# Optimization experiments

Measured on AMD Instinct MI355X. Metric: run time of the kernel, lower is better.

The kernel has to match this reference:

```python
import jax, jax.numpy as jnp
import numpy as np

B, H, N, D = 4, 16, 4096, 64
M = 266  # nb_features = int(D * ln(D))
KERNEL_EPS = 1e-4


def _gaussian_orthogonal_random_matrix(nb_rows, nb_cols, rng):
    # Faithful to gaussian_orthogonal_random_matrix with scaling=0.
    blocks = []
    for _ in range(nb_rows // nb_cols):
        q, _ = np.linalg.qr(rng.standard_normal((nb_cols, nb_cols)))
        blocks.append(q.T)
    rem = nb_rows - (nb_rows // nb_cols) * nb_cols
    if rem > 0:
        q, _ = np.linalg.qr(rng.standard_normal((nb_cols, nb_cols)))
        blocks.append(q.T[:rem])
    final = np.concatenate(blocks, axis=0)
    mult = np.linalg.norm(rng.standard_normal((nb_rows, nb_cols)), axis=1)
    return (mult[:, None] * final).astype(np.float32)


def setup_inputs() -> dict:
    key = jax.random.key(0)
    kq, kk, kv = jax.random.split(key, 3)
    q = jax.random.normal(kq, (B, H, N, D), dtype=jnp.float32)
    k = jax.random.normal(kk, (B, H, N, D), dtype=jnp.float32)
    v = jax.random.normal(kv, (B, H, N, D), dtype=jnp.float32)
    proj = jnp.asarray(_gaussian_orthogonal_random_matrix(M, D, np.random.default_rng(0)))
    return {"q": q, "k": k, "v": v, "projection_matrix": proj}


def _softmax_kernel(x, proj, is_query):
    d = x.shape[-1]
    data_normalizer = d ** (-0.25)
    ratio = proj.shape[0] ** (-0.5)
    # [b,h,n,m]
    data_dash = jnp.einsum("bhnd,md->bhnm", data_normalizer * x, proj)
    diag = jnp.sum(x * x, axis=-1, keepdims=True) * 0.5 * (data_normalizer ** 2)
    if is_query:
        mx = jax.lax.stop_gradient(jnp.max(data_dash, axis=-1, keepdims=True))
    else:
        mx = jax.lax.stop_gradient(jnp.max(data_dash, axis=(-1, -2), keepdims=True))
    return ratio * (jnp.exp(data_dash - diag - mx) + KERNEL_EPS)


def _linear_attention(q, k, v):
    k_cumsum = jnp.sum(k, axis=-2)                       # [b,h,m]
    D_ = jnp.einsum("bhnm,bhm->bhn", q, k_cumsum)
    D_inv = 1.0 / jnp.where(D_ == 0, 1e-5, D_)
    context = jnp.einsum("bhnm,bhne->bhme", k, v)        # [b,h,m,e]
    return jnp.einsum("bhme,bhnm,bhn->bhne", context, q, D_inv)


def reference(q, k, v, projection_matrix):
    qp = _softmax_kernel(q, projection_matrix, is_query=True)
    kp = _softmax_kernel(k, projection_matrix, is_query=False)
    return _linear_attention(qp, kp, v)
```

## Files before the change

kernel.cpp:

```cpp
#include <hip/hip_runtime.h>
#include <math.h>


#define BH 64
#define NTOK 4096
#define DIM 64
#define MF 266
#define MPAD 272
#define NCH 4
#define CHROWS 1024
#define SUBS 16
#define RATIO 0.06131393394849658f
#define DNORM 0.35355339059327373f
#define DIAGC 0.0625f
#define KEPS 1e-4f

#define PSTR 72
#define QSTR 296

typedef _Float16 half8 __attribute__((ext_vector_type(8)));
typedef _Float16 half4 __attribute__((ext_vector_type(4)));
typedef __fp16 fp16x2 __attribute__((ext_vector_type(2)));
typedef float floatx4 __attribute__((ext_vector_type(4)));
typedef short short8 __attribute__((ext_vector_type(8)));
typedef short short4s __attribute__((ext_vector_type(4)));

__device__ __forceinline__ short f2h_bits(float f) {
    union { _Float16 h; short s; } u; u.h = (_Float16)f; return u.s;
}
__device__ __forceinline__ float h2f(short s) {
    union { short s; _Float16 h; } u; u.s = s; return (float)u.h;
}
__device__ __forceinline__ unsigned cvt_pk_bf16(float lo, float hi) {
    unsigned r;
    asm("v_cvt_pk_bf16_f32 %0, %1, %2" : "=v"(r) : "v"(lo), "v"(hi));
    return r;
}
__device__ __forceinline__ unsigned encf(float f) {
    unsigned u = __float_as_uint(f);
    return (u & 0x80000000u) ? ~u : (u | 0x80000000u);
}
__device__ __forceinline__ float decf(unsigned u) {
    u = (u & 0x80000000u) ? (u & 0x7FFFFFFFu) : ~u;
    return __uint_as_float(u);
}

__global__ __launch_bounds__(512, 4)
void k_pass(const float* __restrict__ kin, const float* __restrict__ vin,
            const float* __restrict__ proj, float* __restrict__ A0p,
            float* __restrict__ S0p, unsigned int* __restrict__ gmax)
{
    __shared__ __align__(16) short kL[2][64 * PSTR];
    __shared__ __align__(16) short vT[2][64 * PSTR];
    __shared__ float diagL[2][64];
    __shared__ __align__(16) short epS[16][16 * PSTR];

    const int tid = threadIdx.x;
    const int l = tid & 63, w = tid >> 6;
    const int c = tid & 15, g = (tid >> 4) & 3;
    const int h    = blockIdx.x >> 8;
    const int rest = blockIdx.x & 255;
    const int bh   = rest >> 2;
    const int ch   = rest & 3;
    const int nT = (h == 1 && w == 0) ? 2 : 1;
    const int t0 = (h == 0) ? w : (8 + w);

    half8 pj0[2], pj1[2];
    #pragma unroll
    for (int it = 0; it < 2; ++it) {
        half8 z;
        #pragma unroll
        for (int j = 0; j < 8; ++j) z[j] = (_Float16)0.f;
        pj0[it] = z; pj1[it] = z;
        const int t = it ? 16 : t0;
        const int f = 16 * t + c;
        if (it < nT && f < MF) {
            const float* ps = proj + (size_t)f * 64 + 8 * g;
            float4 x0 = *(const float4*)ps;
            float4 x1 = *(const float4*)(ps + 4);
            float4 x2 = *(const float4*)(ps + 32);
            float4 x3 = *(const float4*)(ps + 36);
            half8 b0, b1;
            b0[0]=(_Float16)(DNORM*x0.x); b0[1]=(_Float16)(DNORM*x0.y);
            b0[2]=(_Float16)(DNORM*x0.z); b0[3]=(_Float16)(DNORM*x0.w);
            b0[4]=(_Float16)(DNORM*x1.x); b0[5]=(_Float16)(DNORM*x1.y);
            b0[6]=(_Float16)(DNORM*x1.z); b0[7]=(_Float16)(DNORM*x1.w);
            b1[0]=(_Float16)(DNORM*x2.x); b1[1]=(_Float16)(DNORM*x2.y);
            b1[2]=(_Float16)(DNORM*x2.z); b1[3]=(_Float16)(DNORM*x2.w);
            b1[4]=(_Float16)(DNORM*x3.x); b1[5]=(_Float16)(DNORM*x3.y);
            b1[6]=(_Float16)(DNORM*x3.z); b1[7]=(_Float16)(DNORM*x3.w);
            pj0[it] = b0; pj1[it] = b1;
        }
    }

    const float* kb = kin + ((size_t)bh * NTOK + (size_t)ch * CHROWS) * DIM;
    const float* vb = vin + ((size_t)bh * NTOK + (size_t)ch * CHROWS) * DIM;

    const int srow = 8 * w + (l >> 3);
    const int sd0  = (l & 7) * 8;
    const int vrow = l;
    const int ve0  = 8 * w;

    floatx4 acc[2][4];
    #pragma unroll
    for (int it = 0; it < 2; ++it)
        #pragma unroll
        for (int et = 0; et < 4; ++et) {
            acc[it][et][0]=0.f; acc[it][et][1]=0.f; acc[it][et][2]=0.f; acc[it][et][3]=0.f;
        }
    float s0acc[2] = {0.f, 0.f};
    float dmax = -3.0e38f;

    float4 ka0, ka1, va0, va1;

    auto issue_loads = [&](int s) {
        const float* ks = kb + (size_t)(64 * s + srow) * DIM + sd0;
        ka0 = *(const float4*)ks;
        ka1 = *(const float4*)(ks + 4);
        const float* vs = vb + (size_t)(64 * s + vrow) * DIM + ve0;
        va0 = *(const float4*)vs;
        va1 = *(const float4*)(vs + 4);
    };

    auto stage_write = [&](int buf) {
        union { fp16x2 h2[4]; short8 s8; } uk;
        uk.h2[0] = __builtin_amdgcn_cvt_pkrtz(ka0.x, ka0.y);
        uk.h2[1] = __builtin_amdgcn_cvt_pkrtz(ka0.z, ka0.w);
        uk.h2[2] = __builtin_amdgcn_cvt_pkrtz(ka1.x, ka1.y);
        uk.h2[3] = __builtin_amdgcn_cvt_pkrtz(ka1.z, ka1.w);
        *(short8*)&kL[buf][srow * PSTR + sd0] = uk.s8;
        float ds2 = ka0.x*ka0.x + ka0.y*ka0.y + ka0.z*ka0.z + ka0.w*ka0.w
                  + ka1.x*ka1.x + ka1.y*ka1.y + ka1.z*ka1.z + ka1.w*ka1.w;
        ds2 += __shfl_xor(ds2, 1);
        ds2 += __shfl_xor(ds2, 2);
        ds2 += __shfl_xor(ds2, 4);
        if ((l & 7) == 0) diagL[buf][srow] = ds2 * DIAGC;
        unsigned pv0 = cvt_pk_bf16(va0.x, va0.y);
        unsigned pv1 = cvt_pk_bf16(va0.z, va0.w);
        unsigned pv2 = cvt_pk_bf16(va1.x, va1.y);
        unsigned pv3 = cvt_pk_bf16(va1.z, va1.w);
        vT[buf][(ve0 + 0) * PSTR + vrow] = (short)(pv0 & 0xFFFF);
        vT[buf][(ve0 + 1) * PSTR + vrow] = (short)(pv0 >> 16);
        vT[buf][(ve0 + 2) * PSTR + vrow] = (short)(pv1 & 0xFFFF);
        vT[buf][(ve0 + 3) * PSTR + vrow] = (short)(pv1 >> 16);
        vT[buf][(ve0 + 4) * PSTR + vrow] = (short)(pv2 & 0xFFFF);
        vT[buf][(ve0 + 5) * PSTR + vrow] = (short)(pv2 >> 16);
        vT[buf][(ve0 + 6) * PSTR + vrow] = (short)(pv3 & 0xFFFF);
        vT[buf][(ve0 + 7) * PSTR + vrow] = (short)(pv3 >> 16);
    };

    issue_loads(0);
    stage_write(0);
    __syncthreads();

    for (int s = 0; s < SUBS; ++s) {
        const int cur = s & 1;
        const bool more = (s + 1 < SUBS);
        if (more) issue_loads(s + 1);

        #pragma unroll
        for (int nt = 0; nt < 4; ++nt) {
            const half8 a0 = *(const half8*)&kL[cur][(16 * nt + c) * PSTR + 8 * g];
            const half8 a1 = *(const half8*)&kL[cur][(16 * nt + c) * PSTR + 8 * g + 32];
            const float4 dg4 = *(const float4*)&diagL[cur][16 * nt + 4 * g];
            const float dgr[4] = {dg4.x, dg4.y, dg4.z, dg4.w};
            #pragma unroll
            for (int it = 0; it < 2; ++it) {
                if (it < nT) {
                    floatx4 d = {0.f, 0.f, 0.f, 0.f};
                    d = __builtin_amdgcn_mfma_f32_16x16x32_f16(a0, pj0[it], d, 0, 0, 0);
                    d = __builtin_amdgcn_mfma_f32_16x16x32_f16(a1, pj1[it], d, 0, 0, 0);
                    const bool t16 = (it == 1);
                    float ev[4];
                    #pragma unroll
                    for (int r = 0; r < 4; ++r) {
                        const float ddv = d[r];
                        if (!t16 || c < 10) dmax = fmaxf(dmax, ddv);
                        float e = __expf(ddv - dgr[r]);
                        if (t16 && c == 15) e = 1.0f;
                        s0acc[it] += e;
                        ev[r] = e;
                    }
                    uint2 pk;
                    pk.x = cvt_pk_bf16(ev[0], ev[1]);
                    pk.y = cvt_pk_bf16(ev[2], ev[3]);
                    *(uint2*)&epS[2 * w + it][c * PSTR + 16 * nt + 4 * g] = pk;
                }
            }
        }

        #pragma unroll
        for (int ntp = 0; ntp < 2; ++ntp) {
            const short8 bq0 = *(const short8*)&epS[2 * w][c * PSTR + 32 * ntp + 8 * g];
            short8 bq1;
            if (nT == 2) bq1 = *(const short8*)&epS[2 * w + 1][c * PSTR + 32 * ntp + 8 * g];
            #pragma unroll
            for (int et = 0; et < 4; ++et) {
                const short8 av = *(const short8*)&vT[cur][(16 * et + c) * PSTR + 32 * ntp + 8 * g];
                acc[0][et] = __builtin_amdgcn_mfma_f32_16x16x32_bf16(av, bq0, acc[0][et], 0, 0, 0);
                if (nT == 2)
                    acc[1][et] = __builtin_amdgcn_mfma_f32_16x16x32_bf16(av, bq1, acc[1][et], 0, 0, 0);
            }
        }

        if (more) {
            stage_write(cur ^ 1);
            __syncthreads();
        }
    }

    {
        float* dst = A0p + (size_t)(bh * NCH + ch) * (MPAD * 64);
        #pragma unroll
        for (int it = 0; it < 2; ++it) {
            if (it < nT) {
                const int t = it ? 16 : t0;
                #pragma unroll
                for (int et = 0; et < 4; ++et)
                    *(floatx4*)&dst[(size_t)(16 * t + c) * 64 + 16 * et + 4 * g] = acc[it][et];
            }
        }
    }
    #pragma unroll
    for (int it = 0; it < 2; ++it) {
        if (it < nT) {
            const int t = it ? 16 : t0;
            float s = s0acc[it];
            s += __shfl_xor(s, 16);
            s += __shfl_xor(s, 32);
            if (g == 0 && (t < 16 || c < 10))
                atomicAdd(&S0p[bh * MPAD + 16 * t + c], s);
        }
    }
    #pragma unroll
    for (int sft = 1; sft <= 32; sft <<= 1) dmax = fmaxf(dmax, __shfl_xor(dmax, sft));
    if (l == 0) atomicMax(gmax + bh, encf(dmax));
}

__global__ __launch_bounds__(512, 1)
void reduce_ctx(const float* __restrict__ A0p, const float* __restrict__ S0p,
                const unsigned int* __restrict__ gmax, const float* __restrict__ proj,
                short* __restrict__ ctxw, short* __restrict__ projw)
{
    __shared__ __align__(16) short L[65 * 288];
    const int bh = blockIdx.x, tid = threadIdx.x;
    if (bh < 17) {
        #pragma unroll
        for (int rep = 0; rep < 2; ++rep) {
            const int idx = rep * 512 + tid;
            const int f = 16 * bh + (idx >> 6);
            const int d = idx & 63;
            const float val = (f < MF) ? proj[(size_t)f * 64 + d] * DNORM : 0.f;
            projw[(size_t)f * 64 + d] = f2h_bits(val);
        }
    }
    const float emx = __expf(-decf(gmax[bh]));
    const int e = tid & 63, mi = tid >> 6;
    const float* base = A0p + (size_t)bh * NCH * MPAD * 64;
    float vs = 0.f;
    #pragma unroll
    for (int c2 = 0; c2 < NCH; ++c2)
        vs += base[(size_t)c2 * MPAD * 64 + (size_t)271 * 64 + e];
    const float vsr = vs * KEPS;
    for (int m = mi; m < 288; m += 8) {
        float val = 0.f;
        if (m < MF) {
            float s = 0.f;
            #pragma unroll
            for (int c2 = 0; c2 < NCH; ++c2)
                s += base[(size_t)c2 * MPAD * 64 + (size_t)m * 64 + e];
            val = RATIO * (emx * s + vsr);
        }
        L[e * 288 + m] = f2h_bits(val);
    }
    for (int m = tid; m < 288; m += 512) {
        float val = 0.f;
        if (m < MF) val = RATIO * (emx * S0p[bh * MPAD + m] + KEPS * 4096.0f);
        L[64 * 288 + m] = f2h_bits(val);
    }
    __syncthreads();
    short* dst = ctxw + (size_t)bh * (65 * 288);
    for (int idx = tid; idx < 65 * 36; idx += 512)
        *(short8*)(dst + idx * 8) = *(const short8*)&L[idx * 8];
}

__global__ __launch_bounds__(512, 2)
void q_pass(const float* __restrict__ qin, const short* __restrict__ projw,
            const short* __restrict__ ctxw, float* __restrict__ outp)
{
    __shared__ __align__(16) short projL[MPAD * PSTR];
    __shared__ __align__(16) short ctxL[65 * QSTR];

    const int tid = threadIdx.x;
    const int bh = blockIdx.x >> 5, rt = blockIdx.x & 31;
    const int c = tid & 15, g = (tid >> 4) & 3, w = tid >> 6;

    for (int idx = tid; idx < MPAD * 8; idx += 512) {
        const int r = idx >> 3, s = idx & 7;
        *(short8*)&projL[r * PSTR + s * 8] = *(const short8*)(projw + (size_t)r * 64 + s * 8);
    }
    {
        const short* src = ctxw + (size_t)bh * (65 * 288);
        for (int idx = tid; idx < 65 * 36; idx += 512) {
            const int r = idx / 36, s = idx - r * 36;
            *(short8*)&ctxL[r * QSTR + s * 8] = *(const short8*)(src + r * 288 + s * 8);
        }
    }
    half8 bf0, bf1;
    float dsum = 0.f;
    {
        const float* qs = qin + ((size_t)bh * NTOK + rt * 128 + 16 * w + c) * DIM;
        #pragma unroll
        for (int ksi = 0; ksi < 2; ++ksi) {
            const float* p4 = qs + ksi * 32 + 8 * g;
            float4 x0 = *(const float4*)p4;
            float4 x1 = *(const float4*)(p4 + 4);
            dsum += x0.x*x0.x + x0.y*x0.y + x0.z*x0.z + x0.w*x0.w
                  + x1.x*x1.x + x1.y*x1.y + x1.z*x1.z + x1.w*x1.w;
            half8& bf = ksi ? bf1 : bf0;
            bf[0]=(_Float16)x0.x; bf[1]=(_Float16)x0.y; bf[2]=(_Float16)x0.z; bf[3]=(_Float16)x0.w;
            bf[4]=(_Float16)x1.x; bf[5]=(_Float16)x1.y; bf[6]=(_Float16)x1.z; bf[7]=(_Float16)x1.w;
        }
    }
    float t1 = dsum + __shfl_xor(dsum, 16);
    const float diagc = (t1 + __shfl_xor(t1, 32)) * DIAGC;

    __syncthreads();

    floatx4 dd[17];
    #pragma unroll
    for (int t = 0; t < 17; ++t) {
        const short* ap = &projL[(16 * t + c) * PSTR + 8 * g];
        half8 a0 = *(const half8*)ap;
        half8 a1 = *(const half8*)(ap + 32);
        floatx4 d = {0.f, 0.f, 0.f, 0.f};
        d = __builtin_amdgcn_mfma_f32_16x16x32_f16(a0, bf0, d, 0, 0, 0);
        d = __builtin_amdgcn_mfma_f32_16x16x32_f16(a1, bf1, d, 0, 0, 0);
        dd[t] = d;
    }
    float mx = -3.0e38f;
    #pragma unroll
    for (int t = 0; t < 17; ++t) {
        #pragma unroll
        for (int r2 = 0; r2 < 4; ++r2) {
            const bool fval = (t < 16) || (4 * g + r2 < 10);
            if (fval) mx = fmaxf(mx, dd[t][r2]);
        }
    }
    mx = fmaxf(mx, __shfl_xor(mx, 16));
    mx = fmaxf(mx, __shfl_xor(mx, 32));

    half4 bq[17];
    float denp = 0.f;
    #pragma unroll
    for (int t = 0; t < 17; ++t) {
        half4 b;
        #pragma unroll
        for (int r2 = 0; r2 < 4; ++r2) {
            float val = __expf(dd[t][r2] - diagc - mx) + KEPS;
            b[r2] = (_Float16)val;
            denp += val * h2f(ctxL[64 * QSTR + 16 * t + 4 * g + r2]);
        }
        bq[t] = b;
    }
    denp += __shfl_xor(denp, 16);
    denp += __shfl_xor(denp, 32);

    floatx4 acc[4];
    #pragma unroll
    for (int i = 0; i < 4; ++i) { acc[i][0]=0.f; acc[i][1]=0.f; acc[i][2]=0.f; acc[i][3]=0.f; }
    #pragma unroll
    for (int e4 = 0; e4 < 4; ++e4) {
        #pragma unroll
        for (int t = 0; t < 17; ++t) {
            half4 a4 = *(const half4*)&ctxL[(16 * e4 + c) * QSTR + 16 * t + 4 * g];
            acc[e4] = __builtin_amdgcn_mfma_f32_16x16x16f16(a4, bq[t], acc[e4], 0, 0, 0);
        }
    }
    float den = (denp == 0.f) ? 1e-5f : denp;
    const float inv = 1.0f / den;
    float* ob = outp + ((size_t)bh * NTOK + rt * 128 + 16 * w + c) * DIM;
    #pragma unroll
    for (int e4 = 0; e4 < 4; ++e4) {
        float4 o = make_float4(acc[e4][0] * inv, acc[e4][1] * inv,
                               acc[e4][2] * inv, acc[e4][3] * inv);
        *(float4*)(ob + 16 * e4 + 4 * g) = o;
    }
}

extern "C" void kernel_launch(void* const* d_in, const int* in_sizes, int n_in,
                              void* d_out, int out_size, void* d_ws, size_t ws_size,
                              hipStream_t stream)
{
    const float* q    = (const float*)d_in[0];
    const float* k    = (const float*)d_in[1];
    const float* v    = (const float*)d_in[2];
    const float* proj = (const float*)d_in[3];
    float* out = (float*)d_out;
    float* ws  = (float*)d_ws;

    const size_t offS = (size_t)BH * NCH * MPAD * 64;
    const size_t offG = offS + (size_t)BH * MPAD;
    const size_t offC = offG + 64;
    const size_t offP = offC + (size_t)BH * 65 * 288 / 2;

    float* A0p = ws;
    float* S0p = ws + offS;
    unsigned int* gmax = (unsigned int*)(ws + offG);
    short* ctxw = (short*)(ws + offC);
    short* projw = (short*)(ws + offP);

    (void)hipMemsetAsync(S0p, 0, ((size_t)BH * MPAD + 64) * sizeof(float), stream);
    hipLaunchKernelGGL(k_pass, dim3(BH * NCH * 2), dim3(512), 0, stream,
                       k, v, proj, A0p, S0p, gmax);
    hipLaunchKernelGGL(reduce_ctx, dim3(BH), dim3(512), 0, stream,
                       A0p, S0p, gmax, proj, ctxw, projw);
    hipLaunchKernelGGL(q_pass, dim3(BH * 32), dim3(512), 0, stream,
                       q, projw, ctxw, out);
}
```

Measured before the change: 132.5 us.

## Recompute projection MFMAs from global to cut registers and LDS in q_pass

Removes the projection-matrix LDS staging from q_pass and reads projection rows directly from global memory. The 17 data_dash tiles are no longer held in registers: the two-MFMA projection is run once for the row max, then recomputed and fused with the exp and context MFMAs in a second pass. Launch bounds rise to 8 waves per SIMD to raise occupancy. In exchange the projection GEMM runs twice, every wave issues uncoalesced-ish global loads for proj, and the tighter register cap may cause spills.

After: 246.1 us. 85.8% more time.

```diff
diff --git a/kernel.cpp b/kernel.cpp
--- a/kernel.cpp
+++ b/kernel.cpp
@@ -284,21 +284,16 @@
         *(short8*)(dst + idx * 8) = *(const short8*)&L[idx * 8];
 }
 
-__global__ __launch_bounds__(512, 2)
+__global__ __launch_bounds__(512, 8)
 void q_pass(const float* __restrict__ qin, const short* __restrict__ projw,
             const short* __restrict__ ctxw, float* __restrict__ outp)
 {
-    __shared__ __align__(16) short projL[MPAD * PSTR];
     __shared__ __align__(16) short ctxL[65 * QSTR];
 
     const int tid = threadIdx.x;
     const int bh = blockIdx.x >> 5, rt = blockIdx.x & 31;
     const int c = tid & 15, g = (tid >> 4) & 3, w = tid >> 6;
 
-    for (int idx = tid; idx < MPAD * 8; idx += 512) {
-        const int r = idx >> 3, s = idx & 7;
-        *(short8*)&projL[r * PSTR + s * 8] = *(const short8*)(projw + (size_t)r * 64 + s * 8);
-    }
     {
         const short* src = ctxw + (size_t)bh * (65 * 288);
         for (int idx = tid; idx < 65 * 36; idx += 512) {
@@ -325,58 +320,55 @@
     float t1 = dsum + __shfl_xor(dsum, 16);
     const float diagc = (t1 + __shfl_xor(t1, 32)) * DIAGC;
 
-    __syncthreads();
-
-    floatx4 dd[17];
+    float mx = -3.0e38f;
     #pragma unroll
     for (int t = 0; t < 17; ++t) {
-        const short* ap = &projL[(16 * t + c) * PSTR + 8 * g];
+        const short* ap = projw + (size_t)(16 * t + c) * 64 + 8 * g;
         half8 a0 = *(const half8*)ap;
         half8 a1 = *(const half8*)(ap + 32);
         floatx4 d = {0.f, 0.f, 0.f, 0.f};
         d = __builtin_amdgcn_mfma_f32_16x16x32_f16(a0, bf0, d, 0, 0, 0);
         d = __builtin_amdgcn_mfma_f32_16x16x32_f16(a1, bf1, d, 0, 0, 0);
-        dd[t] = d;
-    }
-    float mx = -3.0e38f;
-    #pragma unroll
-    for (int t = 0; t < 17; ++t) {
         #pragma unroll
         for (int r2 = 0; r2 < 4; ++r2) {
             const bool fval = (t < 16) || (4 * g + r2 < 10);
-            if (fval) mx = fmaxf(mx, dd[t][r2]);
+            if (fval) mx = fmaxf(mx, d[r2]);
         }
     }
     mx = fmaxf(mx, __shfl_xor(mx, 16));
     mx = fmaxf(mx, __shfl_xor(mx, 32));
 
-    half4 bq[17];
+    __syncthreads();
+
+    floatx4 acc[4];
+    #pragma unroll
+    for (int i = 0; i < 4; ++i) { acc[i][0]=0.f; acc[i][1]=0.f; acc[i][2]=0.f; acc[i][3]=0.f; }
     float denp = 0.f;
     #pragma unroll
     for (int t = 0; t < 17; ++t) {
-        half4 b;
+        const short* ap = projw + (size_t)(16 * t + c) * 64 + 8 * g;
+        half8 a0 = *(const half8*)ap;
+        half8 a1 = *(const half8*)(ap + 32);
+        floatx4 d = {0.f, 0.f, 0.f, 0.f};
+        d = __builtin_amdgcn_mfma_f32_16x16x32_f16(a0, bf0, d, 0, 0, 0);
+        d = __builtin_amdgcn_mfma_f32_16x16x32_f16(a1, bf1, d, 0, 0, 0);
+        half4 bq;
+        const short4s kcs = *(const short4s*)&ctxL[64 * QSTR + 16 * t + 4 * g];
         #pragma unroll
         for (int r2 = 0; r2 < 4; ++r2) {
-            float val = __expf(dd[t][r2] - diagc - mx) + KEPS;
-            b[r2] = (_Float16)val;
-            denp += val * h2f(ctxL[64 * QSTR + 16 * t + 4 * g + r2]);
-        }
-        bq[t] = b;
+            float val = __expf(d[r2] - diagc - mx) + KEPS;
+            bq[r2] = (_Float16)val;
+            denp += val * h2f(kcs[r2]);
+        }
+        #pragma unroll
+        for (int e4 = 0; e4 < 4; ++e4) {
+            half4 a4 = *(const half4*)&ctxL[(16 * e4 + c) * QSTR + 16 * t + 4 * g];
+            acc[e4] = __builtin_amdgcn_mfma_f32_16x16x16f16(a4, bq, acc[e4], 0, 0, 0);
+        }
     }
     denp += __shfl_xor(denp, 16);
     denp += __shfl_xor(denp, 32);
 
-    floatx4 acc[4];
-    #pragma unroll
-    for (int i = 0; i < 4; ++i) { acc[i][0]=0.f; acc[i][1]=0.f; acc[i][2]=0.f; acc[i][3]=0.f; }
-    #pragma unroll
-    for (int e4 = 0; e4 < 4; ++e4) {
-        #pragma unroll
-        for (int t = 0; t < 17; ++t) {
-            half4 a4 = *(const half4*)&ctxL[(16 * e4 + c) * QSTR + 16 * t + 4 * g];
-            acc[e4] = __builtin_amdgcn_mfma_f32_16x16x16f16(a4, bq[t], acc[e4], 0, 0, 0);
-        }
-    }
     float den = (denp == 0.f) ? 1e-5f : denp;
     const float inv = 1.0f / den;
     float* ob = outp + ((size_t)bh * NTOK + rt * 128 + 16 * w + c) * DIM;
```
